# Performance work log

Hardware: AMD Instinct MI355X
Metric: run time of the kernel (lower is better)

Reference implementation:

```python
import jax, jax.numpy as jnp
import numpy as np

N_NODES = 30000
DIM = 128
N_T = 6
N_EDGES = 480000
NEG_SLOPE = 0.2  # GATConv default leaky_relu slope


def _gat(x, src, dst, W, att_src, att_dst, b):
    # PyG GATConv, heads=1, add_self_loops=True, eval mode (no dropout).
    n = x.shape[0]
    loops = jnp.arange(n)
    src = jnp.concatenate([src, loops])
    dst = jnp.concatenate([dst, loops])
    h = x @ W                              # [N, D]
    a_s = h @ att_src                      # [N]
    a_d = h @ att_dst                      # [N]
    e = jax.nn.leaky_relu(a_s[src] + a_d[dst], NEG_SLOPE)   # [E+N]
    m = jax.ops.segment_max(e, dst, num_segments=n)
    ex = jnp.exp(e - m[dst])
    denom = jax.ops.segment_sum(ex, dst, num_segments=n)
    alpha = ex / denom[dst]
    out = jax.ops.segment_sum(h[src] * alpha[:, None], dst, num_segments=n)
    return out + b


def _sage(x, src, dst, Wl, bl, Wr, br):
    # PyG SAGEConv, mean aggregation, root_weight=True.
    n = x.shape[0]
    agg = jax.ops.segment_sum(x[src], dst, num_segments=n)
    cnt = jax.ops.segment_sum(jnp.ones_like(src, dtype=x.dtype), dst, num_segments=n)
    mean = agg / jnp.maximum(cnt, 1.0)[:, None]
    return mean @ Wl + bl + x @ Wr + br


def setup_inputs() -> dict:
    key = jax.random.key(0)
    ks = jax.random.split(key, 16)
    sc = 0.1
    inp = {
        "s": jax.random.randint(ks[0], (1024,), 0, N_NODES),
        "t_s": jax.random.randint(ks[1], (1024,), 0, N_T),
        "t_e": jax.random.randint(ks[2], (1024,), 0, N_T),
        "edge_index": jax.random.randint(ks[3], (N_T, 3, 2, N_EDGES), 0, N_NODES),
        "embed_weight": jax.random.normal(ks[4], (N_NODES, DIM), jnp.float32),
        "W_p": jax.random.normal(ks[5], (DIM, DIM), jnp.float32) * sc,
        "att_src_p": jax.random.normal(ks[6], (DIM,), jnp.float32) * sc,
        "att_dst_p": jax.random.normal(ks[7], (DIM,), jnp.float32) * sc,
        "b_p": jnp.zeros((DIM,), jnp.float32),
        "W_c": jax.random.normal(ks[8], (DIM, DIM), jnp.float32) * sc,
        "att_src_c": jax.random.normal(ks[9], (DIM,), jnp.float32) * sc,
        "att_dst_c": jax.random.normal(ks[10], (DIM,), jnp.float32) * sc,
        "b_c": jnp.zeros((DIM,), jnp.float32),
        "W_l": jax.random.normal(ks[11], (DIM, DIM), jnp.float32) * sc,
        "b_l": jnp.zeros((DIM,), jnp.float32),
        "W_r": jax.random.normal(ks[12], (DIM, DIM), jnp.float32) * sc,
        "b_r": jnp.zeros((DIM,), jnp.float32),
    }
    return inp


def reference(s, t_s, t_e, edge_index, embed_weight,
              W_p, att_src_p, att_dst_p, b_p,
              W_c, att_src_c, att_dst_c, b_c,
              W_l, b_l, W_r, b_r):
    outs = []
    for t in range(N_T):  # fixed small number of timesteps
        ei = edge_index[t]
        gp = _gat(embed_weight, ei[0, 0], ei[0, 1], W_p, att_src_p, att_dst_p, b_p)
        gc = _gat(embed_weight, ei[1, 0], ei[1, 1], W_c, att_src_c, att_dst_c, b_c)
        sg = _sage(embed_weight, ei[2, 0], ei[2, 1], W_l, b_l, W_r, b_r)
        outs.append((gp + gc + sg) / 3.0)  # HeteroConv aggr='mean'
    skill_embs = jnp.stack(outs)           # [n, N, D]
    return skill_embs[:, s, :]             # [n, |s|, D]
```

## Files before the change

kernel.cpp:

```cpp
#include <hip/hip_runtime.h>
#include <hip/hip_bf16.h>

#define NN 30000
#define DIM 128
#define NT 6
#define NE 480000
#define NSLOT 1024
#define NSEG (NT*3*NSLOT)
#define SEGCAP 96
#define NBM ((NN+31)/32)
#define QCAP 2048
#define HB 2048

typedef __attribute__((ext_vector_type(8))) short bf16x8;
typedef __attribute__((ext_vector_type(4))) float f32x4;

__device__ __forceinline__ float lrelu(float x){ return x > 0.f ? x : 0.2f*x; }
__device__ __forceinline__ unsigned short f2b(float f){
    unsigned u = __float_as_uint(f);
    u = (u + 0x7FFFu + ((u>>16)&1u)) >> 16;
    return (unsigned short)u;
}
__device__ __forceinline__ float b2f(unsigned short b){
    return __uint_as_float(((unsigned)b)<<16);
}
__device__ __forceinline__ float blo(unsigned p){ return b2f((unsigned short)(p & 0xFFFF)); }
__device__ __forceinline__ float bhi(unsigned p){ return b2f((unsigned short)(p >> 16)); }
__device__ __forceinline__ unsigned hsh(int v){ return ((unsigned)v*2654435761u >> 21) & (HB-1); }

__global__ void k_prep(const float* __restrict__ Wp, const float* __restrict__ Wc,
        const float* __restrict__ Wl, const float* __restrict__ Wr,
        const float* __restrict__ aspv, const float* __restrict__ adpv,
        const float* __restrict__ ascv, const float* __restrict__ adcv,
        const int* __restrict__ s, unsigned* __restrict__ bm,
        unsigned* __restrict__ hmap, int* __restrict__ rep, int* __restrict__ cnt,
        float* __restrict__ wa, unsigned short* __restrict__ WT4){
    int m = blockIdx.x, t = threadIdx.x;
    if (m >= 5){
        int b = m - 5;
        int per = (NSEG + 7)/8;
        for (int j = b*per + t; j < (b+1)*per && j < NSEG; j += 256) cnt[j] = 0;
        return;
    }
    if (m == 4){
        __shared__ int hk[HB];
        __shared__ int hv[HB];
        __shared__ unsigned bms[NBM];
        for (int j = t; j < HB; j += 256){ hk[j] = -1; hv[j] = 1<<30; }
        for (int j = t; j < NBM; j += 256) bms[j] = 0u;
        __syncthreads();
        for (int i = t; i < NSLOT; i += 256){
            int v = s[i];
            unsigned idx = hsh(v);
            while (true){
                int old = atomicCAS(&hk[idx], -1, v);
                if (old == -1 || old == v){ atomicMin(&hv[idx], i); break; }
                idx = (idx+1)&(HB-1);
            }
            atomicOr(&bms[v>>5], 1u << (v&31));
        }
        __syncthreads();
        for (int j = t; j < NBM; j += 256) bm[j] = bms[j];
        for (int j = t; j < HB; j += 256){
            int k = hk[j];
            hmap[j] = (k < 0) ? 0xFFFFFFFFu : (((unsigned)k << 10) | (unsigned)hv[j]);
        }
        for (int i = t; i < NSLOT; i += 256){
            int v = s[i];
            unsigned idx = hsh(v);
            while (hk[idx] != v) idx = (idx+1)&(HB-1);
            rep[i] = hv[idx];
        }
        return;
    }
    const float* W = (m==0) ? Wp : (m==1) ? Wc : (m==2) ? Wl : Wr;
    unsigned short* WT = WT4 + (size_t)m*DIM*DIM;
    if (m < 2 && t < DIM){
        const float* avs = m ? ascv : aspv;
        const float* avd = m ? adcv : adpv;
        float* wab = wa + m*2*DIM;
        float sv = 0.f, dv = 0.f;
        for (int n = 0; n < DIM; n++){
            float w = W[t*DIM + n];
            sv += w*avs[n]; dv += w*avd[n];
        }
        wab[t] = sv; wab[DIM + t] = dv;
    }
    for (int j = t; j < DIM*DIM; j += blockDim.x){
        int n = j >> 7, k = j & 127;
        WT[n*DIM + k] = f2b(W[k*DIM + n]);
    }
}

__global__ __launch_bounds__(256) void k_cast(const float* __restrict__ X,
        const float* __restrict__ wa, unsigned* __restrict__ Xbf,
        float* __restrict__ asp, float* __restrict__ adp,
        float* __restrict__ asc, float* __restrict__ adc){
    int gw = (blockIdx.x*blockDim.x + threadIdx.x) >> 6;
    int lane = threadIdx.x & 63;
    if (gw >= NN) return;
    float2 x = *(const float2*)&X[(size_t)gw*DIM + lane*2];
    Xbf[(size_t)gw*64 + lane] = (unsigned)f2b(x.x) | ((unsigned)f2b(x.y) << 16);
    float sp = x.x*wa[2*lane]     + x.y*wa[2*lane+1];
    float dp = x.x*wa[128+2*lane] + x.y*wa[128+2*lane+1];
    float sc = x.x*wa[256+2*lane] + x.y*wa[256+2*lane+1];
    float dc = x.x*wa[384+2*lane] + x.y*wa[384+2*lane+1];
    #pragma unroll
    for (int off = 32; off; off >>= 1){
        sp += __shfl_xor(sp, off); dp += __shfl_xor(dp, off);
        sc += __shfl_xor(sc, off); dc += __shfl_xor(dc, off);
    }
    if (lane == 0){ asp[gw] = sp; adp[gw] = dp; asc[gw] = sc; adc[gw] = dc; }
}

__global__ __launch_bounds__(256) void k_build(const int* __restrict__ EI,
        const unsigned* __restrict__ bm, const unsigned* __restrict__ hmap,
        int* __restrict__ cnt, int* __restrict__ csr){
    __shared__ unsigned bms[NBM];
    __shared__ unsigned hm[HB];
    __shared__ unsigned q[QCAP];
    __shared__ int qn;
    for (int j = threadIdx.x; j < NBM; j += 256) bms[j] = bm[j];
    for (int j = threadIdx.x; j < HB; j += 256) hm[j] = hmap[j];
    if (threadIdx.x == 0) qn = 0;
    __syncthreads();
    const int Q = NE/4;
    const int G = gridDim.x*blockDim.x;
    int row = blockIdx.y;
    const int4* dstp = (const int4*)(EI + (size_t)(2*row+1)*NE);
    const int4* srcp = (const int4*)(EI + (size_t)(2*row)*NE);
    int tid = blockIdx.x*blockDim.x + threadIdx.x;
    #pragma unroll
    for (int u = 0; u < 4; u++){
        int ix = tid + u*G;
        if (ix < Q){
            int4 d = dstp[ix];
            unsigned m0 = (bms[d.x>>5] >> (d.x&31)) & 1u;
            unsigned m1 = (bms[d.y>>5] >> (d.y&31)) & 1u;
            unsigned m2 = (bms[d.z>>5] >> (d.z&31)) & 1u;
            unsigned m3 = (bms[d.w>>5] >> (d.w&31)) & 1u;
            if (m0|m1|m2|m3){
                int4 sv = srcp[ix];
                if (m0){ int p = atomicAdd(&qn,1); if (p < QCAP) q[p] = ((unsigned)d.x<<15) | (unsigned)sv.x; }
                if (m1){ int p = atomicAdd(&qn,1); if (p < QCAP) q[p] = ((unsigned)d.y<<15) | (unsigned)sv.y; }
                if (m2){ int p = atomicAdd(&qn,1); if (p < QCAP) q[p] = ((unsigned)d.z<<15) | (unsigned)sv.z; }
                if (m3){ int p = atomicAdd(&qn,1); if (p < QCAP) q[p] = ((unsigned)d.w<<15) | (unsigned)sv.w; }
            }
        }
    }
    __syncthreads();
    int base = row*NSLOT;
    int tot = qn; if (tot > QCAP) tot = QCAP;
    for (int j = threadIdx.x; j < tot; j += 256){
        unsigned e = q[j];
        int dst = (int)(e >> 15);
        int src = (int)(e & 32767u);
        unsigned idx = hsh(dst);
        unsigned he;
        while (((he = hm[idx]) >> 10) != (unsigned)dst) idx = (idx+1)&(HB-1);
        int sl = (int)(he & 1023u);
        int p = atomicAdd(&cnt[base+sl], 1);
        if (p < SEGCAP) csr[(size_t)(base+sl)*SEGCAP + p] = src;
    }
}

__global__ __launch_bounds__(256) void k_aggr(const unsigned* __restrict__ Xbf,
        const float* __restrict__ asp, const float* __restrict__ adp,
        const float* __restrict__ asc, const float* __restrict__ adc,
        const int* __restrict__ s, const int* __restrict__ cnt, const int* __restrict__ csr,
        unsigned* __restrict__ aggb){
    int gw = (blockIdx.x*blockDim.x + threadIdx.x) >> 6;
    int lane = threadIdx.x & 63;
    if (gw >= NSEG) return;
    int slot = gw & (NSLOT-1);
    int tg = gw >> 10;
    int g = tg % 3;
    int n = cnt[gw]; if (n > SEGCAP) n = SEGCAP;
    const int* lst = csr + (size_t)gw*SEGCAP;
    int src0 = (lane < n) ? lst[lane] : 0;
    int src1 = (64+lane < n) ? lst[64+lane] : 0;
    int n0 = n < 64 ? n : 64;
    float w0, w1, wself = 0.f, scale;
    int v = -1;
    if (g == 2){
        w0 = (lane < n) ? 1.f : 0.f;
        w1 = (64+lane < n) ? 1.f : 0.f;
        scale = 1.f / (float)(n > 0 ? n : 1);
    } else {
        const float* as = g ? asc : asp;
        const float* ad = g ? adc : adp;
        v = s[slot];
        float adv = ad[v];
        float eself = lrelu(as[v] + adv);
        float e0 = (lane < n)    ? lrelu(as[src0]+adv) : -3e38f;
        float e1 = (64+lane < n) ? lrelu(as[src1]+adv) : -3e38f;
        float m = fmaxf(eself, fmaxf(e0, e1));
        #pragma unroll
        for (int off = 32; off; off >>= 1) m = fmaxf(m, __shfl_xor(m, off));
        w0 = (lane < n)    ? __expf(e0 - m) : 0.f;
        w1 = (64+lane < n) ? __expf(e1 - m) : 0.f;
        float ds = w0 + w1;
        #pragma unroll
        for (int off = 32; off; off >>= 1) ds += __shfl_xor(ds, off);
        wself = __expf(eself - m);
        scale = 1.f / (wself + ds);
    }
    float a0 = 0.f, a1 = 0.f;
    int j = 0;
    for (; j+3 < n0; j += 4){
        int s0=__shfl(src0,j), s1=__shfl(src0,j+1), s2=__shfl(src0,j+2), s3=__shfl(src0,j+3);
        float q0=__shfl(w0,j), q1=__shfl(w0,j+1), q2=__shfl(w0,j+2), q3=__shfl(w0,j+3);
        unsigned k0=Xbf[(size_t)s0*64+lane];
        unsigned k1=Xbf[(size_t)s1*64+lane];
        unsigned k2=Xbf[(size_t)s2*64+lane];
        unsigned k3=Xbf[(size_t)s3*64+lane];
        a0 += q0*blo(k0) + q1*blo(k1) + q2*blo(k2) + q3*blo(k3);
        a1 += q0*bhi(k0) + q1*bhi(k1) + q2*bhi(k2) + q3*bhi(k3);
    }
    for (; j < n0; j++){
        int sj=__shfl(src0,j);
        float qj=__shfl(w0,j);
        unsigned pk=Xbf[(size_t)sj*64+lane];
        a0 += qj*blo(pk); a1 += qj*bhi(pk);
    }
    for (j = 64; j < n; j++){
        int sj=__shfl(src1,j-64);
        float qj=__shfl(w1,j-64);
        unsigned pk=Xbf[(size_t)sj*64+lane];
        a0 += qj*blo(pk); a1 += qj*bhi(pk);
    }
    if (g < 2){
        unsigned pk = Xbf[(size_t)v*64 + lane];
        a0 += wself*blo(pk); a1 += wself*bhi(pk);
    }
    aggb[(size_t)gw*64 + lane] =
        (unsigned)f2b(a0*scale) | ((unsigned)f2b(a1*scale) << 16);
}

__global__ __launch_bounds__(256) void k_sgemm(const unsigned* __restrict__ aggb,
        const unsigned* __restrict__ Xbf, const unsigned short* __restrict__ WT4,
        const int* __restrict__ s,
        float* __restrict__ aggOut, float* __restrict__ xWr){
    int task = (blockIdx.x >= 288);
    int blk  = task ? (blockIdx.x - 288) : blockIdx.x;
    int wsel = task ? 3 : ((blk >> 4) % 3);
    const unsigned short* WT = WT4 + (size_t)wsel*DIM*DIM;
    float* out = task ? xWr : aggOut;
    int rows = task ? NSLOT : NSEG;
    int wid = threadIdx.x >> 6, lane = threadIdx.x & 63;
    int r0 = blk*64 + wid*16;
    int ar = r0 + (lane & 15); if (ar > rows-1) ar = rows-1;
    int g = lane >> 4;
    const unsigned short* Arow = task
        ? (const unsigned short*)(Xbf + (size_t)s[ar]*64)
        : (const unsigned short*)(aggb + (size_t)ar*64);
    bf16x8 Af[4];
    #pragma unroll
    for (int ks = 0; ks < 4; ks++)
        Af[ks] = *(const bf16x8*)&Arow[ks*32 + g*8];
    int cl = lane & 15;
    #pragma unroll
    for (int ct = 0; ct < 8; ct++){
        f32x4 acc = {0.f,0.f,0.f,0.f};
        int bcol = ct*16 + cl;
        #pragma unroll
        for (int ks = 0; ks < 4; ks++){
            bf16x8 bF = *(const bf16x8*)&WT[bcol*DIM + ks*32 + g*8];
            acc = __builtin_amdgcn_mfma_f32_16x16x32_bf16(Af[ks], bF, acc, 0, 0, 0);
        }
        #pragma unroll
        for (int r = 0; r < 4; r++){
            int row = r0 + g*4 + r;
            if (row < rows) out[(size_t)row*DIM + bcol] = acc[r];
        }
    }
}

__global__ void k_gather(const int* __restrict__ rep,
                         const float* __restrict__ aggOut, const float* __restrict__ xWr,
                         const float* __restrict__ bp, const float* __restrict__ bc,
                         const float* __restrict__ bl, const float* __restrict__ br,
                         float* __restrict__ out){
    int i = blockIdx.x*blockDim.x + threadIdx.x;
    if (i >= NT*NSLOT*DIM) return;
    int d = i & 127;
    int r = (i >> 7) & (NSLOT-1);
    int t = i >> 17;
    int rp = rep[r];
    size_t base = ((size_t)(t*3)*NSLOT + rp)*DIM + d;
    out[i] = (aggOut[base] + aggOut[base + NSLOT*DIM] + aggOut[base + 2*NSLOT*DIM]
              + xWr[(size_t)rp*DIM + d]
              + bp[d] + bc[d] + bl[d] + br[d]) * (1.f/3.f);
}

extern "C" void kernel_launch(void* const* d_in, const int* in_sizes, int n_in,
                              void* d_out, int out_size, void* d_ws, size_t ws_size,
                              hipStream_t stream) {
    const int*   s    = (const int*)d_in[0];
    const int*   EI   = (const int*)d_in[3];
    const float* X    = (const float*)d_in[4];
    const float* Wp   = (const float*)d_in[5];
    const float* aspv = (const float*)d_in[6];
    const float* adpv = (const float*)d_in[7];
    const float* bp   = (const float*)d_in[8];
    const float* Wc   = (const float*)d_in[9];
    const float* ascv = (const float*)d_in[10];
    const float* adcv = (const float*)d_in[11];
    const float* bc   = (const float*)d_in[12];
    const float* Wl   = (const float*)d_in[13];
    const float* bl   = (const float*)d_in[14];
    const float* Wr   = (const float*)d_in[15];
    const float* br   = (const float*)d_in[16];
    float* out = (float*)d_out;

    char* w = (char*)d_ws;
    unsigned* Xbf = (unsigned*)w; w += (size_t)NN*64*4;
    unsigned short* WT4 = (unsigned short*)w; w += (size_t)4*DIM*DIM*2;
    float* wa  = (float*)w; w += (size_t)4*DIM*4;
    float* asp = (float*)w; w += (size_t)NN*4;
    float* adp = (float*)w; w += (size_t)NN*4;
    float* asc = (float*)w; w += (size_t)NN*4;
    float* adc = (float*)w; w += (size_t)NN*4;
    unsigned* bm = (unsigned*)w; w += (size_t)((NBM+3)&~3)*4;
    unsigned* hmap = (unsigned*)w; w += (size_t)HB*4;
    int* rep  = (int*)w; w += (size_t)NSLOT*4;
    int* cnt  = (int*)w; w += (size_t)NSEG*4;
    int* csr  = (int*)w; w += (size_t)NSEG*SEGCAP*4;
    unsigned* aggb = (unsigned*)w; w += (size_t)NSEG*64*4;
    float* aggOut = (float*)w; w += (size_t)NSEG*DIM*4;
    float* xWr = (float*)w; w += (size_t)NSLOT*DIM*4;

    k_prep   <<<13, 256, 0, stream>>>(Wp, Wc, Wl, Wr, aspv, adpv, ascv, adcv,
                                      s, bm, hmap, rep, cnt, wa, WT4);
    k_cast   <<<(NN+3)/4, 256, 0, stream>>>(X, wa, Xbf, asp, adp, asc, adc);
    k_build  <<<dim3(118, 18), 256, 0, stream>>>(EI, bm, hmap, cnt, csr);
    k_aggr   <<<NSEG/4, 256, 0, stream>>>(Xbf, asp, adp, asc, adc, s, cnt, csr, aggb);
    k_sgemm  <<<304, 256, 0, stream>>>(aggb, Xbf, WT4, s, aggOut, xWr);
    k_gather <<<NT*NSLOT*DIM/256, 256, 0, stream>>>(rep, aggOut, xWr, bp, bc, bl, br, out);
}
```

Baseline: 91.27 us.

## Batch edge loads, wave-aggregate queue atomics, drop LDS hash copy, unroll gather by 8

In k_build, all four int4 destination loads are now issued before any bitmap checks, giving more memory-level parallelism. Per-lane LDS atomics on the queue counter are replaced by one ballot-based atomic per wavefront. The 8KB shared-memory copy of the hash map is removed and probes read it from global memory instead, which cuts LDS setup and usage but adds global-latency probes. In k_aggr, an 8-way unrolled gather loop puts more loads in flight.

```diff
diff --git a/kernel.cpp b/kernel.cpp
--- a/kernel.cpp
+++ b/kernel.cpp
@@ -117,11 +117,9 @@
         const unsigned* __restrict__ bm, const unsigned* __restrict__ hmap,
         int* __restrict__ cnt, int* __restrict__ csr){
     __shared__ unsigned bms[NBM];
-    __shared__ unsigned hm[HB];
     __shared__ unsigned q[QCAP];
     __shared__ int qn;
     for (int j = threadIdx.x; j < NBM; j += 256) bms[j] = bm[j];
-    for (int j = threadIdx.x; j < HB; j += 256) hm[j] = hmap[j];
     if (threadIdx.x == 0) qn = 0;
     __syncthreads();
     const int Q = NE/4;
@@ -130,21 +128,45 @@
     const int4* dstp = (const int4*)(EI + (size_t)(2*row+1)*NE);
     const int4* srcp = (const int4*)(EI + (size_t)(2*row)*NE);
     int tid = blockIdx.x*blockDim.x + threadIdx.x;
+    int lane = threadIdx.x & 63;
+
+    int4 d[4]; int ix[4]; bool va[4];
     #pragma unroll
     for (int u = 0; u < 4; u++){
-        int ix = tid + u*G;
-        if (ix < Q){
-            int4 d = dstp[ix];
-            unsigned m0 = (bms[d.x>>5] >> (d.x&31)) & 1u;
-            unsigned m1 = (bms[d.y>>5] >> (d.y&31)) & 1u;
-            unsigned m2 = (bms[d.z>>5] >> (d.z&31)) & 1u;
-            unsigned m3 = (bms[d.w>>5] >> (d.w&31)) & 1u;
-            if (m0|m1|m2|m3){
-                int4 sv = srcp[ix];
-                if (m0){ int p = atomicAdd(&qn,1); if (p < QCAP) q[p] = ((unsigned)d.x<<15) | (unsigned)sv.x; }
-                if (m1){ int p = atomicAdd(&qn,1); if (p < QCAP) q[p] = ((unsigned)d.y<<15) | (unsigned)sv.y; }
-                if (m2){ int p = atomicAdd(&qn,1); if (p < QCAP) q[p] = ((unsigned)d.z<<15) | (unsigned)sv.z; }
-                if (m3){ int p = atomicAdd(&qn,1); if (p < QCAP) q[p] = ((unsigned)d.w<<15) | (unsigned)sv.w; }
+        ix[u] = tid + u*G;
+        va[u] = ix[u] < Q;
+        d[u] = va[u] ? dstp[ix[u]] : make_int4(0,0,0,0);
+    }
+    unsigned mk[4];
+    #pragma unroll
+    for (int u = 0; u < 4; u++){
+        unsigned m0 = va[u] ? ((bms[d[u].x>>5] >> (d[u].x&31)) & 1u) : 0u;
+        unsigned m1 = va[u] ? ((bms[d[u].y>>5] >> (d[u].y&31)) & 1u) : 0u;
+        unsigned m2 = va[u] ? ((bms[d[u].z>>5] >> (d[u].z&31)) & 1u) : 0u;
+        unsigned m3 = va[u] ? ((bms[d[u].w>>5] >> (d[u].w&31)) & 1u) : 0u;
+        mk[u] = m0 | (m1<<1) | (m2<<2) | (m3<<3);
+    }
+    int4 sv[4];
+    #pragma unroll
+    for (int u = 0; u < 4; u++)
+        if (mk[u]) sv[u] = srcp[ix[u]];
+    #pragma unroll
+    for (int u = 0; u < 4; u++){
+        #pragma unroll
+        for (int c = 0; c < 4; c++){
+            bool p = (mk[u] >> c) & 1u;
+            unsigned long long bal = __ballot(p);
+            if (bal){
+                int cntw = __popcll(bal);
+                int base = 0;
+                if (lane == 0) base = atomicAdd(&qn, cntw);
+                base = __shfl(base, 0);
+                if (p){
+                    int dv = (c==0)?d[u].x:(c==1)?d[u].y:(c==2)?d[u].z:d[u].w;
+                    int so = (c==0)?sv[u].x:(c==1)?sv[u].y:(c==2)?sv[u].z:sv[u].w;
+                    int pos = base + __popcll(bal & ((1ull<<lane)-1ull));
+                    if (pos < QCAP) q[pos] = ((unsigned)dv<<15) | (unsigned)so;
+                }
             }
         }
     }
@@ -157,7 +179,7 @@
         int src = (int)(e & 32767u);
         unsigned idx = hsh(dst);
         unsigned he;
-        while (((he = hm[idx]) >> 10) != (unsigned)dst) idx = (idx+1)&(HB-1);
+        while (((he = hmap[idx]) >> 10) != (unsigned)dst) idx = (idx+1)&(HB-1);
         int sl = (int)(he & 1023u);
         int p = atomicAdd(&cnt[base+sl], 1);
         if (p < SEGCAP) csr[(size_t)(base+sl)*SEGCAP + p] = src;
@@ -207,6 +229,15 @@
     }
     float a0 = 0.f, a1 = 0.f;
     int j = 0;
+    for (; j+7 < n0; j += 8){
+        int   si[8]; float qi[8]; unsigned ki[8];
+        #pragma unroll
+        for (int u = 0; u < 8; u++){ si[u] = __shfl(src0, j+u); qi[u] = __shfl(w0, j+u); }
+        #pragma unroll
+        for (int u = 0; u < 8; u++) ki[u] = Xbf[(size_t)si[u]*64 + lane];
+        #pragma unroll
+        for (int u = 0; u < 8; u++){ a0 += qi[u]*blo(ki[u]); a1 += qi[u]*bhi(ki[u]); }
+    }
     for (; j+3 < n0; j += 4){
         int s0=__shfl(src0,j), s1=__shfl(src0,j+1), s2=__shfl(src0,j+2), s3=__shfl(src0,j+3);
         float q0=__shfl(w0,j), q1=__shfl(w0,j+1), q2=__shfl(w0,j+2), q3=__shfl(w0,j+3);
```

Result: faster. 84.68 us (-7.2%).
